# Optimization experiments

Hardware: AMD Instinct MI355X
Metric: run time of the kernel (lower is better)

## Reference

```python
import jax, jax.numpy as jnp
import numpy as np

R_DISC = 0.05  # radius for discrepancy indicator
R_SIM = 0.03   # radius for sim/cross (indicator computed but unused downstream, as in source)
EPS = 1e-9


def setup_inputs() -> dict:
    key = jax.random.key(0)
    k1, k2, k3, k4 = jax.random.split(key, 4)
    bz, N, nsmp, K, C = 32, 16384, 4096, 64, 6
    features = jax.random.normal(k1, (bz, N, C), dtype=jnp.float32)
    nearest_k_idx = jax.random.randint(k2, (bz, nsmp, K), 0, N)
    # distances in [0, 0.06) so roughly half fall within r=0.03/0.05
    nearest_k_dist = jax.random.uniform(k3, (bz, nsmp, K), dtype=jnp.float32) * 0.06
    fps_idx = jax.random.randint(k4, (bz * nsmp,), 0, bz * N)
    return {"features": features, "nearest_k_idx": nearest_k_idx,
            "nearest_k_dist": nearest_k_dist, "fps_idx": fps_idx}


def _batched_index_select(features, idx):
    # features [bz,N,C], idx [bz,nsmp,K] -> [bz,nsmp,K,C]
    return jax.vmap(lambda f, i: f[i])(features, idx)


def _cos_sim_avg(feat_sub, nk_feat):
    # feat_sub [bz,nsmp,d], nk_feat [bz,nsmp,K,d] -> [bz,nsmp,1]
    num = jnp.sum(feat_sub[:, :, None, :] * nk_feat, axis=-1)
    den = jnp.maximum(jnp.linalg.norm(feat_sub, axis=-1)[:, :, None]
                      * jnp.linalg.norm(nk_feat, axis=-1), EPS)
    return jnp.mean(num / den, axis=-1, keepdims=True)


def reference(features, nearest_k_idx, nearest_k_dist, fps_idx):
    bz, N, C = features.shape
    nsmp = nearest_k_idx.shape[1]
    nk = _batched_index_select(features, nearest_k_idx)          # [bz,nsmp,K,C]
    feats_sub = features.reshape(bz * N, C)[fps_idx].reshape(bz, nsmp, C)

    # --- generate_feature_discrepancy (r=0.05): masked weighted neighbor mean ---
    ind = (nearest_k_dist <= R_DISC).astype(features.dtype)[..., None]  # [bz,nsmp,K,1]
    nk_avg = jnp.sum(nk * ind, axis=2) / jnp.sum(ind, axis=2)
    discrepancy = feats_sub - nk_avg                              # [bz,nsmp,C]

    # --- generate_feature_sim (r=0.03): mean cosine sim on xyz and normal splits ---
    sim = jnp.concatenate([_cos_sim_avg(feats_sub[:, :, :3], nk[:, :, :, :3]),
                           _cos_sim_avg(feats_sub[:, :, 3:], nk[:, :, :, 3:])],
                          axis=-1)                                # [bz,nsmp,2]

    # --- generate_feature_cross_prod: mean of feat_sub x neighbor over K ---
    cross = jnp.cross(feats_sub[:, :, None, :3], nk[:, :, :, :3])  # [bz,nsmp,K,3]
    cross_avg = jnp.mean(cross, axis=2)                            # [bz,nsmp,3]

    return jnp.concatenate([discrepancy, sim, cross_avg], axis=-1)  # [bz,nsmp,C+5]
```

## Files before the change

kernel.cpp:

```cpp
#include <hip/hip_runtime.h>

#define BZ    32
#define NPTS  16384
#define NSMP  4096
#define KNB   64
#define NCH   6
#define RDISC 0.05f
#define EPSV  1e-9f


__global__ __launch_bounds__(256) void pnpp_kernel(
    const float* __restrict__ feat,
    const int*   __restrict__ nk_idx,
    const float* __restrict__ nk_dist,
    const int*   __restrict__ fps_idx,
    float*       __restrict__ out)
{
    const int lane = threadIdx.x & 63;
    const int wid  = threadIdx.x >> 6;
    const int bid  = blockIdx.x;
    const int work = (bid & 7) * (gridDim.x >> 3) + (bid >> 3);
    const int g = lane >> 4;
    const int j = lane & 15;
    const int s = work * 16 + wid * 4 + g;
    const int b = s >> 12;

    const long kbase = (long)s * KNB + j * 4;
    const int4   idx4 = *(const int4*)  (nk_idx  + kbase);
    const float4 dst4 = *(const float4*)(nk_dist + kbase);

    const int p = fps_idx[s];
    const float* fsrow = feat + (long)p * NCH;
    const float2 a01 = *(const float2*)(fsrow);
    const float2 a23 = *(const float2*)(fsrow + 2);
    const float2 a45 = *(const float2*)(fsrow + 4);
    const float fs0 = a01.x, fs1 = a01.y, fs2 = a23.x;
    const float fs3 = a23.y, fs4 = a45.x, fs5 = a45.y;
    const float nfs1 = sqrtf(fs0*fs0 + fs1*fs1 + fs2*fs2);
    const float nfs2 = sqrtf(fs3*fs3 + fs4*fs4 + fs5*fs5);

    const float* fb = feat + (long)b * (NPTS * NCH);

    float cnt = 0.f;
    float s0=0.f,s1=0.f,s2=0.f,s3=0.f,s4=0.f,s5=0.f;
    float c1=0.f, c2=0.f;
    float cr0=0.f, cr1=0.f, cr2=0.f;

    const int   idxs[4] = {idx4.x, idx4.y, idx4.z, idx4.w};
    const float dsts[4] = {dst4.x, dst4.y, dst4.z, dst4.w};

    #pragma unroll
    for (int q = 0; q < 4; ++q) {
        const float* fr = fb + (long)idxs[q] * NCH;
        const float2 f01 = *(const float2*)(fr);
        const float2 f23 = *(const float2*)(fr + 2);
        const float2 f45 = *(const float2*)(fr + 4);
        const float f0=f01.x, f1=f01.y, f2=f23.x, f3=f23.y, f4=f45.x, f5=f45.y;

        const float ind = (dsts[q] <= RDISC) ? 1.f : 0.f;
        cnt += ind;
        s0 += ind*f0; s1 += ind*f1; s2 += ind*f2;
        s3 += ind*f3; s4 += ind*f4; s5 += ind*f5;

        const float num1 = fs0*f0 + fs1*f1 + fs2*f2;
        const float nf1  = sqrtf(f0*f0 + f1*f1 + f2*f2);
        c1 += num1 / fmaxf(nfs1 * nf1, EPSV);

        const float num2 = fs3*f3 + fs4*f4 + fs5*f5;
        const float nf2  = sqrtf(f3*f3 + f4*f4 + f5*f5);
        c2 += num2 / fmaxf(nfs2 * nf2, EPSV);

        cr0 += fs1*f2 - fs2*f1;
        cr1 += fs2*f0 - fs0*f2;
        cr2 += fs0*f1 - fs1*f0;
    }

    #pragma unroll
    for (int m = 1; m < 16; m <<= 1) {
        cnt += __shfl_xor(cnt, m, 64);
        s0  += __shfl_xor(s0,  m, 64);
        s1  += __shfl_xor(s1,  m, 64);
        s2  += __shfl_xor(s2,  m, 64);
        s3  += __shfl_xor(s3,  m, 64);
        s4  += __shfl_xor(s4,  m, 64);
        s5  += __shfl_xor(s5,  m, 64);
        c1  += __shfl_xor(c1,  m, 64);
        c2  += __shfl_xor(c2,  m, 64);
        cr0 += __shfl_xor(cr0, m, 64);
        cr1 += __shfl_xor(cr1, m, 64);
        cr2 += __shfl_xor(cr2, m, 64);
    }

    const float rc = 1.f / cnt;
    const float d0 = fs0 - s0*rc, d1 = fs1 - s1*rc, d2 = fs2 - s2*rc;
    const float d3 = fs3 - s3*rc, d4 = fs4 - s4*rc, d5 = fs5 - s5*rc;
    const float inv_k = 1.f / (float)KNB;
    const float o6 = c1 * inv_k, o7 = c2 * inv_k;
    const float o8 = cr0 * inv_k, o9 = cr1 * inv_k, o10 = cr2 * inv_k;

    float o = d0;
    o = (j == 1)  ? d1  : o;
    o = (j == 2)  ? d2  : o;
    o = (j == 3)  ? d3  : o;
    o = (j == 4)  ? d4  : o;
    o = (j == 5)  ? d5  : o;
    o = (j == 6)  ? o6  : o;
    o = (j == 7)  ? o7  : o;
    o = (j == 8)  ? o8  : o;
    o = (j == 9)  ? o9  : o;
    o = (j == 10) ? o10 : o;
    if (j < 11) out[(long)s * 11 + j] = o;
}

extern "C" void kernel_launch(void* const* d_in, const int* in_sizes, int n_in,
                              void* d_out, int out_size, void* d_ws, size_t ws_size,
                              hipStream_t stream) {
    const float* feat = (const float*)d_in[0];
    const int*   nki  = (const int*)  d_in[1];
    const float* nkd  = (const float*)d_in[2];
    const int*   fps  = (const int*)  d_in[3];
    float* out = (float*)d_out;

    const int total_samples = BZ * NSMP;
    const int blocks = total_samples / 16;
    pnpp_kernel<<<dim3(blocks), dim3(256), 0, stream>>>(feat, nki, nkd, fps, out);
}
```

Before: 50.64 us.

## Assign four lanes per sample, factor cross product, use rsq for cosine

Remaps work so each sample is handled by 4 lanes processing 16 neighbors each, with 64-thread blocks and a shorter shuffle reduction. The averaged cross product is computed once from the mean neighbor xyz instead of per neighbor. Cosine similarity uses a hardware reciprocal square root of the product of squared norms instead of sqrt and divide, which drops the epsilon clamp. Feature rows are read with wider vector loads. The aim is to cut ALU and reduction overhead and raise per-thread loads in flight, at the cost of fewer threads and possible NaN for zero-norm vectors.

```diff
diff --git a/kernel.cpp b/kernel.cpp
--- a/kernel.cpp
+++ b/kernel.cpp
@@ -6,10 +6,9 @@
 #define KNB   64
 #define NCH   6
 #define RDISC 0.05f
-#define EPSV  1e-9f
 
 
-__global__ __launch_bounds__(256) void pnpp_kernel(
+__global__ __launch_bounds__(64) void pnpp_kernel(
     const float* __restrict__ feat,
     const int*   __restrict__ nk_idx,
     const float* __restrict__ nk_dist,
@@ -17,66 +16,60 @@
     float*       __restrict__ out)
 {
     const int lane = threadIdx.x & 63;
-    const int wid  = threadIdx.x >> 6;
     const int bid  = blockIdx.x;
     const int work = (bid & 7) * (gridDim.x >> 3) + (bid >> 3);
-    const int g = lane >> 4;
-    const int j = lane & 15;
-    const int s = work * 16 + wid * 4 + g;
+    const int g = lane >> 2;
+    const int j = lane & 3;
+    const int s = work * 16 + g;
     const int b = s >> 12;
-
-    const long kbase = (long)s * KNB + j * 4;
-    const int4   idx4 = *(const int4*)  (nk_idx  + kbase);
-    const float4 dst4 = *(const float4*)(nk_dist + kbase);
 
     const int p = fps_idx[s];
     const float* fsrow = feat + (long)p * NCH;
-    const float2 a01 = *(const float2*)(fsrow);
-    const float2 a23 = *(const float2*)(fsrow + 2);
-    const float2 a45 = *(const float2*)(fsrow + 4);
-    const float fs0 = a01.x, fs1 = a01.y, fs2 = a23.x;
-    const float fs3 = a23.y, fs4 = a45.x, fs5 = a45.y;
-    const float nfs1 = sqrtf(fs0*fs0 + fs1*fs1 + fs2*fs2);
-    const float nfs2 = sqrtf(fs3*fs3 + fs4*fs4 + fs5*fs5);
+    const float4 fa  = *(const float4*)(fsrow);
+    const float2 fb2 = *(const float2*)(fsrow + 4);
+    const float fs0=fa.x, fs1=fa.y, fs2=fa.z, fs3=fa.w, fs4=fb2.x, fs5=fb2.y;
+    const float qs1 = fs0*fs0 + fs1*fs1 + fs2*fs2;
+    const float qs2 = fs3*fs3 + fs4*fs4 + fs5*fs5;
 
-    const float* fb = feat + (long)b * (NPTS * NCH);
+    const float* fbase = feat + (long)b * (NPTS * NCH);
 
-    float cnt = 0.f;
+    float cnt=0.f;
     float s0=0.f,s1=0.f,s2=0.f,s3=0.f,s4=0.f,s5=0.f;
-    float c1=0.f, c2=0.f;
-    float cr0=0.f, cr1=0.f, cr2=0.f;
+    float m0=0.f,m1=0.f,m2=0.f;
+    float c1=0.f,c2=0.f;
 
-    const int   idxs[4] = {idx4.x, idx4.y, idx4.z, idx4.w};
-    const float dsts[4] = {dst4.x, dst4.y, dst4.z, dst4.w};
+    const long kb0 = (long)s * KNB + j * 4;
+    #pragma unroll
+    for (int c = 0; c < 4; ++c) {
+        const int4   i4 = *(const int4*)  (nk_idx  + kb0 + c * 16);
+        const float4 d4 = *(const float4*)(nk_dist + kb0 + c * 16);
+        const int   ridx[4] = {i4.x, i4.y, i4.z, i4.w};
+        const float rdst[4] = {d4.x, d4.y, d4.z, d4.w};
+        #pragma unroll
+        for (int q = 0; q < 4; ++q) {
+            const float* fr = fbase + (long)ridx[q] * NCH;
+            const float4 fA = *(const float4*)(fr);
+            const float2 fB = *(const float2*)(fr + 4);
+            const float f0=fA.x, f1=fA.y, f2=fA.z, f3=fA.w, f4=fB.x, f5=fB.y;
 
-    #pragma unroll
-    for (int q = 0; q < 4; ++q) {
-        const float* fr = fb + (long)idxs[q] * NCH;
-        const float2 f01 = *(const float2*)(fr);
-        const float2 f23 = *(const float2*)(fr + 2);
-        const float2 f45 = *(const float2*)(fr + 4);
-        const float f0=f01.x, f1=f01.y, f2=f23.x, f3=f23.y, f4=f45.x, f5=f45.y;
+            const float ind = (rdst[q] <= RDISC) ? 1.f : 0.f;
+            cnt += ind;
+            s0 += ind*f0; s1 += ind*f1; s2 += ind*f2;
+            s3 += ind*f3; s4 += ind*f4; s5 += ind*f5;
+            m0 += f0; m1 += f1; m2 += f2;
 
-        const float ind = (dsts[q] <= RDISC) ? 1.f : 0.f;
-        cnt += ind;
-        s0 += ind*f0; s1 += ind*f1; s2 += ind*f2;
-        s3 += ind*f3; s4 += ind*f4; s5 += ind*f5;
+            const float q1 = f0*f0 + f1*f1 + f2*f2;
+            const float n1 = fs0*f0 + fs1*f1 + fs2*f2;
+            c1 += n1 * __builtin_amdgcn_rsqf(qs1 * q1);
 
-        const float num1 = fs0*f0 + fs1*f1 + fs2*f2;
-        const float nf1  = sqrtf(f0*f0 + f1*f1 + f2*f2);
-        c1 += num1 / fmaxf(nfs1 * nf1, EPSV);
-
-        const float num2 = fs3*f3 + fs4*f4 + fs5*f5;
-        const float nf2  = sqrtf(f3*f3 + f4*f4 + f5*f5);
-        c2 += num2 / fmaxf(nfs2 * nf2, EPSV);
-
-        cr0 += fs1*f2 - fs2*f1;
-        cr1 += fs2*f0 - fs0*f2;
-        cr2 += fs0*f1 - fs1*f0;
+            const float q2 = f3*f3 + f4*f4 + f5*f5;
+            const float n2 = fs3*f3 + fs4*f4 + fs5*f5;
+            c2 += n2 * __builtin_amdgcn_rsqf(qs2 * q2);
+        }
     }
 
     #pragma unroll
-    for (int m = 1; m < 16; m <<= 1) {
+    for (int m = 1; m < 4; m <<= 1) {
         cnt += __shfl_xor(cnt, m, 64);
         s0  += __shfl_xor(s0,  m, 64);
         s1  += __shfl_xor(s1,  m, 64);
@@ -84,32 +77,30 @@
         s3  += __shfl_xor(s3,  m, 64);
         s4  += __shfl_xor(s4,  m, 64);
         s5  += __shfl_xor(s5,  m, 64);
+        m0  += __shfl_xor(m0,  m, 64);
+        m1  += __shfl_xor(m1,  m, 64);
+        m2  += __shfl_xor(m2,  m, 64);
         c1  += __shfl_xor(c1,  m, 64);
         c2  += __shfl_xor(c2,  m, 64);
-        cr0 += __shfl_xor(cr0, m, 64);
-        cr1 += __shfl_xor(cr1, m, 64);
-        cr2 += __shfl_xor(cr2, m, 64);
     }
 
-    const float rc = 1.f / cnt;
+    const float rc = __builtin_amdgcn_rcpf(cnt);
     const float d0 = fs0 - s0*rc, d1 = fs1 - s1*rc, d2 = fs2 - s2*rc;
     const float d3 = fs3 - s3*rc, d4 = fs4 - s4*rc, d5 = fs5 - s5*rc;
-    const float inv_k = 1.f / (float)KNB;
-    const float o6 = c1 * inv_k, o7 = c2 * inv_k;
-    const float o8 = cr0 * inv_k, o9 = cr1 * inv_k, o10 = cr2 * inv_k;
+    const float ik = 1.f / (float)KNB;
+    const float o6 = c1 * ik, o7 = c2 * ik;
+    const float mm0 = m0 * ik, mm1 = m1 * ik, mm2 = m2 * ik;
+    const float o8  = fs1*mm2 - fs2*mm1;
+    const float o9  = fs2*mm0 - fs0*mm2;
+    const float o10 = fs0*mm1 - fs1*mm0;
 
-    float o = d0;
-    o = (j == 1)  ? d1  : o;
-    o = (j == 2)  ? d2  : o;
-    o = (j == 3)  ? d3  : o;
-    o = (j == 4)  ? d4  : o;
-    o = (j == 5)  ? d5  : o;
-    o = (j == 6)  ? o6  : o;
-    o = (j == 7)  ? o7  : o;
-    o = (j == 8)  ? o8  : o;
-    o = (j == 9)  ? o9  : o;
-    o = (j == 10) ? o10 : o;
-    if (j < 11) out[(long)s * 11 + j] = o;
+    const float v0 = (j==0) ? d0 : (j==1) ? d1 : (j==2) ? d2 : d3;
+    const float v1 = (j==0) ? d4 : (j==1) ? d5 : (j==2) ? o6 : o7;
+    const float v2 = (j==0) ? o8 : (j==1) ? o9 : o10;
+    float* orow = out + (long)s * 11;
+    orow[j]     = v0;
+    orow[4 + j] = v1;
+    if (j < 3) orow[8 + j] = v2;
 }
 
 extern "C" void kernel_launch(void* const* d_in, const int* in_sizes, int n_in,
@@ -123,5 +114,5 @@
 
     const int total_samples = BZ * NSMP;
     const int blocks = total_samples / 16;
-    pnpp_kernel<<<dim3(blocks), dim3(256), 0, stream>>>(feat, nki, nkd, fps, out);
+    pnpp_kernel<<<dim3(blocks), dim3(64), 0, stream>>>(feat, nki, nkd, fps, out);
 }
```

Result: slower. 54.41 us (+7.4%).
